# Optimization experiments

Measured on AMD Instinct MI355X. Metric: run time of the kernel, lower is better.

The kernel has to match this reference:

```python
import jax, jax.numpy as jnp
import numpy as np
from jax import lax


def _phi(x):
    # feature map phi(x) = elu(x) + 1 (non-negative)
    return jax.nn.elu(x) + 1.0


def setup_inputs() -> dict:
    key = jax.random.key(0)
    ks = jax.random.split(key, 5)
    B, T, D, H = 8, 4096, 1024, 64
    x = jax.random.normal(ks[0], (B, T, D), dtype=jnp.float32)
    # torch Linear(d_model, d_head, bias=False): y = x @ W.T; store as (in, out)
    W_q = jax.random.normal(ks[1], (D, H), dtype=jnp.float32) * (1.0 / np.sqrt(D))
    W_k = jax.random.normal(ks[2], (D, H), dtype=jnp.float32) * (1.0 / np.sqrt(D))
    W_v = jax.random.normal(ks[3], (D, H), dtype=jnp.float32) * (1.0 / np.sqrt(D))
    W_o = jax.random.normal(ks[4], (H, D), dtype=jnp.float32) * (1.0 / np.sqrt(H))
    return {"x": x, "W_q": W_q, "W_k": W_k, "W_v": W_v, "W_o": W_o}


def reference(x, W_q, W_k, W_v, W_o):
    B, T, D = x.shape
    H = W_q.shape[1]
    q = _phi(jnp.einsum('btd,dh->bth', x, W_q))  # [B,T,H]
    k = _phi(jnp.einsum('btd,dh->bth', x, W_k))
    v = jnp.einsum('btd,dh->bth', x, W_v)

    # time-major for scan: [T,B,H]
    qT = jnp.swapaxes(q, 0, 1)
    kT = jnp.swapaxes(k, 0, 1)
    vT = jnp.swapaxes(v, 0, 1)

    S0 = jnp.zeros((B, H, H), dtype=x.dtype)
    z0 = jnp.zeros((B, H), dtype=x.dtype)

    def step(carry, inp):
        S, z = carry
        q_t, k_t, v_t = inp
        S = S + k_t[:, :, None] * v_t[:, None, :]   # S += phi(k) v^T
        z = z + k_t
        o_t = jnp.einsum('bij,bj->bi', S, q_t)       # matches torch einsum exactly
        denom = jnp.maximum(jnp.sum(z * q_t, axis=-1, keepdims=True), 1e-6)
        return (S, z), o_t / denom

    (_, _), oT = lax.scan(step, (S0, z0), (qT, kT, vT))  # oT: [T,B,H]
    o = jnp.swapaxes(oT, 0, 1)                            # [B,T,H]
    # dropout is identity at inference
    return jnp.einsum('bth,hd->btd', o, W_o)
```

## Files before the change

kernel.cpp:

```cpp
#include <hip/hip_runtime.h>
#include <math.h>

typedef float4 f4;
typedef __attribute__((ext_vector_type(4))) float f32x4;
typedef __attribute__((ext_vector_type(8))) short short8;
typedef __attribute__((ext_vector_type(4))) unsigned short u16x4;

static constexpr int kB  = 8;
static constexpr int kT  = 4096;
static constexpr int kD  = 1024;
static constexpr int kH  = 64;
static constexpr int kC  = 64;
static constexpr int kNC = kT / kC;
static constexpr long kBT = (long)kB * kT;

__device__ __forceinline__ float phi_f(float x) {
    return x > 0.0f ? x + 1.0f : __expf(x);
}

__device__ __forceinline__ unsigned short f2bf(float f) {
    unsigned int u = __float_as_uint(f);
    u += 0x7FFF + ((u >> 16) & 1);
    return (unsigned short)(u >> 16);
}

typedef const __attribute__((address_space(1))) unsigned int gu32;
typedef __attribute__((address_space(3))) unsigned int lu32;
#define GLL16(SRC, DST) __builtin_amdgcn_global_load_lds((gu32*)(SRC), (lu32*)(DST), 16, 0, 0)

#define LD4F(dst, src) { f4 _t_ = *(const f4*)(src); (dst)[0]=_t_.x; (dst)[1]=_t_.y; (dst)[2]=_t_.z; (dst)[3]=_t_.w; }

__global__ __launch_bounds__(256)
void k0_prep(const float* __restrict__ Wq, const float* __restrict__ Wk,
             const float* __restrict__ Wv, const float* __restrict__ Wo,
             unsigned short* __restrict__ Wt, unsigned short* __restrict__ Wot)
{
    int g = blockIdx.x * 256 + threadIdx.x;
    if (g < 12288) {
        int n  = g >> 6;
        int kc = (g & 63) * 16;
        int mat = n >> 6, nn = n & 63;
        const float* W = (mat == 0) ? Wq : ((mat == 1) ? Wk : Wv);
        unsigned short* dst = Wt + (long)n * kD + kc;
        #pragma unroll
        for (int i = 0; i < 16; ++i) dst[i] = f2bf(W[(long)(kc + i) * kH + nn]);
    } else if (g < 12288 + 4096) {
        int g2 = g - 12288;
        int n  = g2 >> 2;
        int kc = (g2 & 3) * 16;
        unsigned short* dst = Wot + n * kH + kc;
        #pragma unroll
        for (int i = 0; i < 16; ++i) dst[i] = f2bf(Wo[(long)(kc + i) * kD + n]);
    }
}

__global__ __launch_bounds__(256, 4)
void k1_qkv_mfma(const float* __restrict__ x, const unsigned short* __restrict__ Wt,
                 float* __restrict__ q, float* __restrict__ k, float* __restrict__ v)
{
    __shared__ unsigned short As[64 * 32];
    __shared__ unsigned short Bs[192 * 32];

    const int t = threadIdx.x;
    const int w = t >> 6;
    const int l = t & 63;
    const long mb = (long)blockIdx.x * 64;

    f32x4 acc[12];
    #pragma unroll
    for (int i = 0; i < 12; ++i) acc[i] = (f32x4){0.f, 0.f, 0.f, 0.f};

    const int arow = t >> 2;
    const int ach  = t & 3;
    const float* aptr = x + (mb + arow) * kD + ach * 8;
    unsigned short* adst = As + arow * 32 + ((ach ^ (arow & 3)) * 8);

    const int brow_in = l >> 2;
    const int bch     = l & 3;

    const int am_row = w * 16 + (l & 15);
    const unsigned short* afp = As + am_row * 32 + (((l >> 4) ^ (am_row & 3)) * 8);

    f32x4 a0 = *(const f32x4*)aptr;
    f32x4 a1 = *(const f32x4*)(aptr + 4);

    for (int k0 = 0; k0 < kD; k0 += 32) {
        #pragma unroll
        for (int c = 0; c < 3; ++c) {
            int r = (c * 4 + w) * 16 + brow_in;
            int g = bch ^ (r & 3);
            GLL16(Wt + (long)r * kD + k0 + g * 8, Bs + (c * 4 + w) * 512);
        }
        short8 ab;
        ab[0] = (short)f2bf(a0[0]); ab[1] = (short)f2bf(a0[1]);
        ab[2] = (short)f2bf(a0[2]); ab[3] = (short)f2bf(a0[3]);
        ab[4] = (short)f2bf(a1[0]); ab[5] = (short)f2bf(a1[1]);
        ab[6] = (short)f2bf(a1[2]); ab[7] = (short)f2bf(a1[3]);
        *(short8*)adst = ab;
        if (k0 + 32 < kD) {
            a0 = *(const f32x4*)(aptr + k0 + 32);
            a1 = *(const f32x4*)(aptr + k0 + 36);
        }
        __syncthreads();

        short8 af = *(const short8*)afp;
        #pragma unroll
        for (int n16 = 0; n16 < 12; ++n16) {
            int r = n16 * 16 + (l & 15);
            short8 bf = *(const short8*)(Bs + r * 32 + (((l >> 4) ^ (r & 3)) * 8));
            acc[n16] = __builtin_amdgcn_mfma_f32_16x16x32_bf16(af, bf, acc[n16], 0, 0, 0);
        }
        __syncthreads();
    }

    const int om = (l >> 4) * 4;
    #pragma unroll
    for (int n16 = 0; n16 < 12; ++n16) {
        int mat = n16 >> 2;
        int col = (n16 & 3) * 16 + (l & 15);
        float* outp = (mat == 0) ? q : ((mat == 1) ? k : v);
        #pragma unroll
        for (int reg = 0; reg < 4; ++reg) {
            long row = mb + w * 16 + om + reg;
            float val = acc[n16][reg];
            if (mat < 2) val = phi_f(val);
            outp[row * kH + col] = val;
        }
    }
}

__global__ __launch_bounds__(256)
void k2_state(const float* __restrict__ k, const float* __restrict__ v,
              float* __restrict__ Sc, float* __restrict__ zc)
{
    __shared__ float Ks2[64][64];
    __shared__ float Vs2[64][64];
    const int t = threadIdx.x;
    const long bc = blockIdx.x;
    const long rowbase = bc * kC;

    #pragma unroll
    for (int i = 0; i < 4; ++i) {
        int fi  = t + i * 256;
        int tau = fi >> 4;
        int cc  = (fi & 15) * 4;
        *(f4*)&Ks2[tau][cc] = *(const f4*)&k[(rowbase + tau) * kH + cc];
        *(f4*)&Vs2[tau][cc] = *(const f4*)&v[(rowbase + tau) * kH + cc];
    }
    __syncthreads();

    const int i  = t >> 2;
    const int j0 = (t & 3) * 16;
    float acc[16];
    #pragma unroll
    for (int c = 0; c < 16; ++c) acc[c] = 0.0f;
    float zacc = 0.0f;

    for (int tau = 0; tau < 64; ++tau) {
        float kv = Ks2[tau][i];
        zacc += kv;
        #pragma unroll
        for (int c = 0; c < 4; ++c) {
            float vv[4];
            LD4F(vv, &Vs2[tau][j0 + c * 4]);
            #pragma unroll
            for (int e = 0; e < 4; ++e) acc[c * 4 + e] += kv * vv[e];
        }
    }
    float* scp = Sc + bc * (kH * kH) + i * kH + j0;
    #pragma unroll
    for (int c = 0; c < 4; ++c) {
        f4 val; val.x = acc[c*4]; val.y = acc[c*4+1]; val.z = acc[c*4+2]; val.w = acc[c*4+3];
        *(f4*)&scp[c * 4] = val;
    }
    if ((t & 3) == 0) zc[bc * kH + i] = zacc;
}

__global__ __launch_bounds__(256)
void k3_prefix(const float* __restrict__ Sc, float* __restrict__ Sp,
               const float* __restrict__ zc, float* __restrict__ zp)
{
    const int t = threadIdx.x;
    const int blk = blockIdx.x;
    if (blk < 128) {
        int g = blk * 256 + t;
        int b = g >> 12;
        int rem = g & 4095;
        const float* src = Sc + (long)b * kNC * kH * kH + rem;
        float*       dst = Sp + (long)b * kNC * kH * kH + rem;
        float vals[kNC];
        #pragma unroll
        for (int c = 0; c < kNC; ++c) vals[c] = src[c * (kH * kH)];
        float run = 0.0f;
        #pragma unroll
        for (int c = 0; c < kNC; ++c) { float nv = vals[c]; vals[c] = run; run += nv; }
        #pragma unroll
        for (int c = 0; c < kNC; ++c) dst[c * (kH * kH)] = vals[c];
    } else {
        int g = (blk - 128) * 256 + t;
        int b = g >> 6;
        int i = g & 63;
        const float* src = zc + (long)b * kNC * kH + i;
        float*       dst = zp + (long)b * kNC * kH + i;
        float vals[kNC];
        #pragma unroll
        for (int c = 0; c < kNC; ++c) vals[c] = src[c * kH];
        float run = 0.0f;
        #pragma unroll
        for (int c = 0; c < kNC; ++c) { float nv = vals[c]; vals[c] = run; run += nv; }
        #pragma unroll
        for (int c = 0; c < kNC; ++c) dst[c * kH] = vals[c];
    }
}

__global__ __launch_bounds__(256)
void k4_chunkout(const float* __restrict__ q, const float* __restrict__ k,
                 const float* __restrict__ v, const float* __restrict__ Sp,
                 const float* __restrict__ zp, unsigned short* __restrict__ o)
{
    __shared__ float QT[64 * 64];
    __shared__ float KsS[64 * 64];
    __shared__ float VT[64 * 64];
    __shared__ float zps[64];
    __shared__ float ds[64];

    const int t = threadIdx.x;
    const long bc = blockIdx.x;
    const long rowbase = bc * kC;

    #pragma unroll
    for (int ii = 0; ii < 4; ++ii) {
        int fi  = t + ii * 256;
        int tau = fi >> 4;
        int c4  = fi & 15;
        f4 qv = *(const f4*)&q[(rowbase + tau) * kH + c4 * 4];
        QT[(c4 * 4 + 0) * 64 + tau] = qv.x;
        QT[(c4 * 4 + 1) * 64 + tau] = qv.y;
        QT[(c4 * 4 + 2) * 64 + tau] = qv.z;
        QT[(c4 * 4 + 3) * 64 + tau] = qv.w;
        f4 vv = *(const f4*)&v[(rowbase + tau) * kH + c4 * 4];
        VT[(c4 * 4 + 0) * 64 + tau] = vv.x;
        VT[(c4 * 4 + 1) * 64 + tau] = vv.y;
        VT[(c4 * 4 + 2) * 64 + tau] = vv.z;
        VT[(c4 * 4 + 3) * 64 + tau] = vv.w;
        f4 kv = *(const f4*)&k[(rowbase + tau) * kH + c4 * 4];
        *(f4*)&KsS[tau * 64 + 4 * (c4 ^ (tau & 15))] = kv;
    }
    if (t < 16) {
        *(f4*)&zps[t * 4] = *(const f4*)&zp[bc * kH + t * 4];
    }
    __syncthreads();

    const int tg   = t & 15;
    const int ig   = t >> 4;
    const int tau0 = tg * 4;
    const int ip0  = ig * 4;

    float pv[4][4];
    #pragma unroll
    for (int a = 0; a < 4; ++a)
        #pragma unroll
        for (int b2 = 0; b2 < 4; ++b2) pv[a][b2] = 0.0f;
    for (int xx = 0; xx < 64; ++xx) {
        float q4[4], v4[4];
        LD4F(q4, &QT[xx * 64 + tau0]);
        LD4F(v4, &VT[xx * 64 + ip0]);
        #pragma unroll
        for (int e1 = 0; e1 < 4; ++e1)
            #pragma unroll
            for (int e0 = 0; e0 < 4; ++e0) pv[e1][e0] += v4[e1] * q4[e0];
    }
    __syncthreads();
    #pragma unroll
    for (int e1 = 0; e1 < 4; ++e1) {
        int tp = ip0 + e1;
        f4 w;
        w.x = (tp <= tau0 + 0) ? pv[e1][0] : 0.0f;
        w.y = (tp <= tau0 + 1) ? pv[e1][1] : 0.0f;
        w.z = (tp <= tau0 + 2) ? pv[e1][2] : 0.0f;
        w.w = (tp <= tau0 + 3) ? pv[e1][3] : 0.0f;
        *(f4*)&VT[tp * 64 + tau0] = w;
    }
    __syncthreads();

    float acc[4][4];
    #pragma unroll
    for (int a = 0; a < 4; ++a)
        #pragma unroll
        for (int b2 = 0; b2 < 4; ++b2) acc[a][b2] = 0.0f;
    for (int tp = 0; tp < 64; ++tp) {
        float p4[4], k4[4];
        LD4F(p4, &VT[tp * 64 + tau0]);
        LD4F(k4, &KsS[tp * 64 + 4 * (ig ^ (tp & 15))]);
        #pragma unroll
        for (int e0 = 0; e0 < 4; ++e0)
            #pragma unroll
            for (int e1 = 0; e1 < 4; ++e1) acc[e0][e1] += p4[e0] * k4[e1];
    }
    __syncthreads();

    #pragma unroll
    for (int ii = 0; ii < 4; ++ii) {
        int fi = t + ii * 256;
        int ir = fi >> 4;
        int j4 = fi & 15;
        f4 sv = *(const f4*)&Sp[bc * (kH * kH) + ir * kH + j4 * 4];
        VT[(j4 * 4 + 0) * 64 + ir] = sv.x;
        VT[(j4 * 4 + 1) * 64 + ir] = sv.y;
        VT[(j4 * 4 + 2) * 64 + ir] = sv.z;
        VT[(j4 * 4 + 3) * 64 + ir] = sv.w;
    }
    if (t < 64) {
        float run = 0.0f;
        const int jc4 = t >> 2, jr = t & 3;
        for (int tau = 0; tau < 64; ++tau) {
            int idx = tau * 64 + 4 * (jc4 ^ (tau & 15)) + jr;
            run += KsS[idx];
            KsS[idx] = run;
        }
    }
    __syncthreads();

    if (t < 64) {
        float dacc = 0.0f;
        for (int j = 0; j < 64; ++j) {
            float qv = QT[j * 64 + t];
            float ck = KsS[t * 64 + 4 * ((j >> 2) ^ (t & 15)) + (j & 3)];
            dacc += qv * (ck + zps[j]);
        }
        ds[t] = 1.0f / fmaxf(dacc, 1e-6f);
    }

    for (int j = 0; j < 64; ++j) {
        float q4[4], s4[4];
        LD4F(q4, &QT[j * 64 + tau0]);
        LD4F(s4, &VT[j * 64 + ip0]);
        #pragma unroll
        for (int e0 = 0; e0 < 4; ++e0)
            #pragma unroll
            for (int e1 = 0; e1 < 4; ++e1) acc[e0][e1] += q4[e0] * s4[e1];
    }
    __syncthreads();

    #pragma unroll
    for (int e0 = 0; e0 < 4; ++e0) {
        float inv = ds[tau0 + e0];
        u16x4 wv;
        wv[0] = f2bf(acc[e0][0] * inv);
        wv[1] = f2bf(acc[e0][1] * inv);
        wv[2] = f2bf(acc[e0][2] * inv);
        wv[3] = f2bf(acc[e0][3] * inv);
        *(u16x4*)&o[(rowbase + tau0 + e0) * kH + ip0] = wv;
    }
}

__global__ __launch_bounds__(256, 4)
void k5_outproj_mfma(const unsigned short* __restrict__ o,
                     const unsigned short* __restrict__ Wot,
                     float* __restrict__ out)
{
    __shared__ unsigned short Os[128 * 64];
    __shared__ unsigned short Ws5[128 * 64];
    const int t = threadIdx.x;
    const int w = t >> 6, l = t & 63;
    const int wm = w >> 1, wn = w & 1;
    const int mb = blockIdx.x >> 3;
    const int nb = blockIdx.x & 7;
    const long row0 = (long)mb * 128;
    const int  col0 = nb * 128;

    const int rin = l >> 3;
    const int cch = l & 7;
    #pragma unroll
    for (int c = 0; c < 4; ++c) {
        int r = (c * 4 + w) * 8 + rin;
        int g = cch ^ (r & 7);
        GLL16(o   + (row0 + r) * kH + g * 8,        Os  + (c * 4 + w) * 512);
        GLL16(Wot + (long)(col0 + r) * kH + g * 8,  Ws5 + (c * 4 + w) * 512);
    }
    __syncthreads();

    short8 af[4][2];
    #pragma unroll
    for (int mf = 0; mf < 4; ++mf) {
        int ar = wm * 64 + mf * 16 + (l & 15);
        #pragma unroll
        for (int ks = 0; ks < 2; ++ks)
            af[mf][ks] = *(const short8*)(Os + ar * 64 + (((ks * 4 + (l >> 4)) ^ (ar & 7)) * 8));
    }

    f32x4 acc[4][4];
    #pragma unroll
    for (int a = 0; a < 4; ++a)
        #pragma unroll
        for (int b2 = 0; b2 < 4; ++b2) acc[a][b2] = (f32x4){0.f, 0.f, 0.f, 0.f};

    #pragma unroll
    for (int nf = 0; nf < 4; ++nf) {
        int br = wn * 64 + nf * 16 + (l & 15);
        short8 bf0 = *(const short8*)(Ws5 + br * 64 + ((((l >> 4)) ^ (br & 7)) * 8));
        short8 bf1 = *(const short8*)(Ws5 + br * 64 + (((4 + (l >> 4)) ^ (br & 7)) * 8));
        #pragma unroll
        for (int mf = 0; mf < 4; ++mf) {
            acc[mf][nf] = __builtin_amdgcn_mfma_f32_16x16x32_bf16(af[mf][0], bf0, acc[mf][nf], 0, 0, 0);
            acc[mf][nf] = __builtin_amdgcn_mfma_f32_16x16x32_bf16(af[mf][1], bf1, acc[mf][nf], 0, 0, 0);
        }
    }

    #pragma unroll
    for (int mf = 0; mf < 4; ++mf)
        #pragma unroll
        for (int nf = 0; nf < 4; ++nf) {
            #pragma unroll
            for (int reg = 0; reg < 4; ++reg) {
                long row = row0 + wm * 64 + mf * 16 + (l >> 4) * 4 + reg;
                int  col = col0 + wn * 64 + nf * 16 + (l & 15);
                out[row * kD + col] = acc[mf][nf][reg];
            }
        }
}

extern "C" void kernel_launch(void* const* d_in, const int* in_sizes, int n_in,
                              void* d_out, int out_size, void* d_ws, size_t ws_size,
                              hipStream_t stream)
{
    const float* x  = (const float*)d_in[0];
    const float* Wq = (const float*)d_in[1];
    const float* Wk = (const float*)d_in[2];
    const float* Wv = (const float*)d_in[3];
    const float* Wo = (const float*)d_in[4];
    float* out = (float*)d_out;
    float* ws  = (float*)d_ws;

    const long NQ = kBT * kH;
    float* q  = ws;
    float* k  = ws + NQ;
    float* v  = ws + 2 * NQ;
    float* Sc = ws + 3 * NQ;
    float* Sp = ws + 4 * NQ;
    unsigned short* obf = (unsigned short*)(ws + 5 * NQ);
    float* zc = ws + 5 * NQ + NQ / 2;
    float* zp = zc + (long)kB * kNC * kH;
    unsigned short* Wt  = (unsigned short*)(zp + (long)kB * kNC * kH);
    unsigned short* Wot = Wt + 192 * 1024;

    k0_prep<<<64, 256, 0, stream>>>(Wq, Wk, Wv, Wo, Wt, Wot);
    k1_qkv_mfma<<<512, 256, 0, stream>>>(x, Wt, q, k, v);
    k2_state<<<kB * kNC, 256, 0, stream>>>(k, v, Sc, zc);
    k3_prefix<<<130, 256, 0, stream>>>(Sc, Sp, zc, zp);
    k4_chunkout<<<kB * kNC, 256, 0, stream>>>(q, k, v, Sp, zp, obf);
    k5_outproj_mfma<<<2048, 256, 0, stream>>>(obf, Wot, out);
}
```

Baseline: 317.6 us.

## Drop LDS staging in QKV GEMM and load MFMA fragments directly from global

```diff
diff --git a/kernel.cpp b/kernel.cpp
--- a/kernel.cpp
+++ b/kernel.cpp
@@ -54,63 +54,39 @@
     }
 }
 
-__global__ __launch_bounds__(256, 4)
+__global__ __launch_bounds__(256, 2)
 void k1_qkv_mfma(const float* __restrict__ x, const unsigned short* __restrict__ Wt,
                  float* __restrict__ q, float* __restrict__ k, float* __restrict__ v)
 {
-    __shared__ unsigned short As[64 * 32];
-    __shared__ unsigned short Bs[192 * 32];
-
     const int t = threadIdx.x;
     const int w = t >> 6;
     const int l = t & 63;
     const long mb = (long)blockIdx.x * 64;
 
+    const int  lrow = l & 15;
+    const int  kch  = (l >> 4) * 8;
+
+    const float*          ap = x  + (mb + w * 16 + lrow) * kD + kch;
+    const unsigned short* bp = Wt + (long)lrow * kD + kch;
+
     f32x4 acc[12];
     #pragma unroll
     for (int i = 0; i < 12; ++i) acc[i] = (f32x4){0.f, 0.f, 0.f, 0.f};
 
-    const int arow = t >> 2;
-    const int ach  = t & 3;
-    const float* aptr = x + (mb + arow) * kD + ach * 8;
-    unsigned short* adst = As + arow * 32 + ((ach ^ (arow & 3)) * 8);
-
-    const int brow_in = l >> 2;
-    const int bch     = l & 3;
-
-    const int am_row = w * 16 + (l & 15);
-    const unsigned short* afp = As + am_row * 32 + (((l >> 4) ^ (am_row & 3)) * 8);
-
-    f32x4 a0 = *(const f32x4*)aptr;
-    f32x4 a1 = *(const f32x4*)(aptr + 4);
-
+    #pragma unroll 4
     for (int k0 = 0; k0 < kD; k0 += 32) {
-        #pragma unroll
-        for (int c = 0; c < 3; ++c) {
-            int r = (c * 4 + w) * 16 + brow_in;
-            int g = bch ^ (r & 3);
-            GLL16(Wt + (long)r * kD + k0 + g * 8, Bs + (c * 4 + w) * 512);
-        }
-        short8 ab;
-        ab[0] = (short)f2bf(a0[0]); ab[1] = (short)f2bf(a0[1]);
-        ab[2] = (short)f2bf(a0[2]); ab[3] = (short)f2bf(a0[3]);
-        ab[4] = (short)f2bf(a1[0]); ab[5] = (short)f2bf(a1[1]);
-        ab[6] = (short)f2bf(a1[2]); ab[7] = (short)f2bf(a1[3]);
-        *(short8*)adst = ab;
-        if (k0 + 32 < kD) {
-            a0 = *(const f32x4*)(aptr + k0 + 32);
-            a1 = *(const f32x4*)(aptr + k0 + 36);
-        }
-        __syncthreads();
-
-        short8 af = *(const short8*)afp;
+        f32x4 a0 = *(const f32x4*)(ap + k0);
+        f32x4 a1 = *(const f32x4*)(ap + k0 + 4);
+        short8 af;
+        af[0] = (short)f2bf(a0[0]); af[1] = (short)f2bf(a0[1]);
+        af[2] = (short)f2bf(a0[2]); af[3] = (short)f2bf(a0[3]);
+        af[4] = (short)f2bf(a1[0]); af[5] = (short)f2bf(a1[1]);
+        af[6] = (short)f2bf(a1[2]); af[7] = (short)f2bf(a1[3]);
         #pragma unroll
         for (int n16 = 0; n16 < 12; ++n16) {
-            int r = n16 * 16 + (l & 15);
-            short8 bf = *(const short8*)(Bs + r * 32 + (((l >> 4) ^ (r & 3)) * 8));
+            short8 bf = *(const short8*)(bp + (long)n16 * 16 * kD + k0);
             acc[n16] = __builtin_amdgcn_mfma_f32_16x16x32_bf16(af, bf, acc[n16], 0, 0, 0);
         }
-        __syncthreads();
     }
 
     const int om = (l >> 4) * 4;
```

Result: slower. 382.2 us (+20.3%).
